# Kernel tuning notes

Hardware: AMD Instinct MI355X
Metric: run time of the kernel (lower is better)

Reference implementation:

```python
import jax, jax.numpy as jnp
import numpy as np
from jax import lax

B, N, NP, NS, CIN = 4, 8192, 2048, 32, 64
RADIUS = 0.1
CH = [CIN + 3, 64, 64, 128]  # mlp[0] += 3 because use_xyz=True
EPS = 1e-5


def _gather(x, idx):
    # x: [B, N, D], idx: [B, ...] int -> [B, ..., D]
    return jax.vmap(lambda a, i: a[i])(x, idx)


def _fps(xyz, npoint):
    # furthest point sampling, returns indices [B, npoint]
    b, n, _ = xyz.shape
    init_idx = jnp.zeros((b,), jnp.int32)
    dist0 = jnp.full((b, n), 1e10, xyz.dtype)

    def body(carry, _):
        dist, last = carry
        p = jnp.take_along_axis(xyz, last[:, None, None], axis=1)  # [B,1,3]
        d = jnp.sum((xyz - p) ** 2, axis=-1)                       # [B,N]
        dist = jnp.minimum(dist, d)
        nxt = jnp.argmax(dist, axis=-1).astype(jnp.int32)
        return (dist, nxt), nxt

    (_, _), rest = lax.scan(body, (dist0, init_idx), None, length=npoint - 1)
    return jnp.concatenate([init_idx[None, :], rest], axis=0).T    # [B, npoint]


def _ball_query(xyz, new_xyz, radius, nsample):
    # first `nsample` points within radius; pad with the first hit (0 if none)
    n = xyz.shape[1]
    d2 = jnp.sum((new_xyz[:, :, None, :] - xyz[:, None, :, :]) ** 2, axis=-1)  # [B,NP,N]
    score = jnp.where(d2 < radius * radius, jnp.arange(n, dtype=jnp.int32), n)
    neg_vals, _ = lax.top_k(-score, nsample)   # smallest indices first
    idx = -neg_vals                            # [B,NP,nsample]
    first = idx[..., :1]
    fill = jnp.where(first >= n, 0, first)
    return jnp.where(idx >= n, fill, idx)


def setup_inputs() -> dict:
    key = jax.random.key(0)
    ks = jax.random.split(key, 16)
    inp = {
        "xyz": jax.random.uniform(ks[0], (B, N, 3), jnp.float32),
        "features": jax.random.normal(ks[1], (B, CIN, N), jnp.float32),
    }
    for i in range(3):
        ci, co = CH[i], CH[i + 1]
        inp[f"W{i}"] = jax.random.normal(ks[2 + 4 * i], (co, ci), jnp.float32) / np.sqrt(ci)
        inp[f"b{i}"] = jnp.zeros((co,), jnp.float32)
        inp[f"g{i}"] = jnp.ones((co,), jnp.float32)
        inp[f"beta{i}"] = jnp.zeros((co,), jnp.float32)
    return inp


def _forward(xyz, features, params):
    fps_idx = _fps(xyz, NP)
    new_xyz = _gather(xyz, fps_idx)                                 # [B,NP,3]
    idx = _ball_query(xyz, new_xyz, RADIUS, NS)                     # [B,NP,NS]
    g_xyz = _gather(xyz, idx) - new_xyz[:, :, None, :]              # relative xyz
    g_feat = _gather(jnp.swapaxes(features, 1, 2), idx)             # [B,NP,NS,CIN]
    h = jnp.concatenate([g_xyz, g_feat], axis=-1)                   # [B,NP,NS,3+CIN]
    for (W, b, g, be) in params:
        h = jnp.einsum('bpsc,oc->bpso', h, W) + b                   # 1x1 conv
        mu = jnp.mean(h, axis=(0, 1, 2))
        var = jnp.var(h, axis=(0, 1, 2))
        h = (h - mu) * lax.rsqrt(var + EPS) * g + be                # BatchNorm2d (batch stats)
        h = jax.nn.relu(h)
    new_features = jnp.max(h, axis=2)                               # max-pool over nsample
    return new_xyz, jnp.swapaxes(new_features, 1, 2)                # [B,Cout,NP]


def reference(xyz, features, W0, b0, g0, beta0, W1, b1, g1, beta1, W2, b2, g2, beta2):
    params = ((W0, b0, g0, beta0), (W1, b1, g1, beta1), (W2, b2, g2, beta2))
    return _forward(xyz, features, params)
```

## Files before the change

kernel.cpp:

```cpp
#include <hip/hip_runtime.h>
#include <hip/hip_bf16.h>
#include <cstdint>

#define B_   4
#define N_   8192
#define NP_  2048
#define NS_  32
#define CIN_ 64
#define M_   (B_*NP_*NS_)
#define EPS_ 1e-5f
#define R2_  0.01f

typedef unsigned long long ull;
typedef float v2f __attribute__((ext_vector_type(2)));

__global__ __launch_bounds__(256) void transpose_kernel(const float* __restrict__ feat,
                                                        __hip_bfloat16* __restrict__ featT)
{
    __shared__ float tile[64][65];
    const int b  = blockIdx.y;
    const int j0 = blockIdx.x * 64;
    const int tx = threadIdx.x & 63, ty = threadIdx.x >> 6;
    for (int cc = ty; cc < 64; cc += 4)
        tile[tx][cc] = feat[((size_t)(b*CIN_ + cc))*N_ + j0 + tx];
    __syncthreads();
    for (int cc = ty; cc < 64; cc += 4)
        featT[((size_t)(b*N_ + j0 + cc))*64 + tx] = __float2bfloat16(tile[cc][tx]);
}

template<int CTRL>
__device__ __forceinline__ float dppmaxf(float v)
{
    int o = __builtin_amdgcn_update_dpp(__float_as_int(v), __float_as_int(v), CTRL, 0xF, 0xF, false);
    return fmaxf(v, __int_as_float(o));
}

__global__ __launch_bounds__(512) void fps_kernel(const float* __restrict__ xyz,
    int* __restrict__ fps_idx, float* __restrict__ new_xyzf, float* __restrict__ out)
{
#pragma clang fp contract(off)
    const int b = blockIdx.x;
    const int t = threadIdx.x;
    const float* X = xyz + (size_t)b * N_ * 3;

    __shared__ float xs[N_], ys[N_], zs[N_];
    __shared__ float wavemax[8];
    __shared__ unsigned widx_slot[2];

    for (int p = t; p < N_; p += 512) {
        xs[p] = X[p*3+0]; ys[p] = X[p*3+1]; zs[p] = X[p*3+2];
    }
    if (t < 2) widx_slot[t] = 0u;

    v2f px[8], py[8], pz[8], dst[8];
#pragma unroll
    for (int g = 0; g < 8; ++g) {
        const int p0 = (2*g)*512 + t, p1 = (2*g+1)*512 + t;
        px[g] = (v2f){X[p0*3+0], X[p1*3+0]};
        py[g] = (v2f){X[p0*3+1], X[p1*3+1]};
        pz[g] = (v2f){X[p0*3+2], X[p1*3+2]};
        dst[g] = (v2f){1e10f, 1e10f};
    }
    const int wv = t >> 6, ln = t & 63;

    float cx = X[0], cy = X[1], cz = X[2];
    if (t == 0) {
        fps_idx[b*NP_] = 0;
        size_t o3 = (size_t)(b*NP_) * 3;
        new_xyzf[o3] = cx; new_xyzf[o3+1] = cy; new_xyzf[o3+2] = cz;
        out[o3] = cx; out[o3+1] = cy; out[o3+2] = cz;
    }
    for (int it = 1; it < NP_; ++it) {
        const int par = it & 1;
        float bestv = -1.0f;
        const v2f c0 = (v2f){cx, cx}, c1 = (v2f){cy, cy}, c2 = (v2f){cz, cz};
#pragma unroll
        for (int g = 0; g < 8; ++g) {
            v2f dx = px[g] - c0, dy = py[g] - c1, dz = pz[g] - c2;
            v2f dd = dx*dx;
            dd = dd + dy*dy;
            dd = dd + dz*dz;
            v2f nd;
            nd.x = fminf(dst[g].x, dd.x);
            nd.y = fminf(dst[g].y, dd.y);
            dst[g] = nd;
            bestv = fmaxf(bestv, nd.x);
            bestv = fmaxf(bestv, nd.y);
        }
        float wm = bestv;
        wm = dppmaxf<0x111>(wm);
        wm = dppmaxf<0x112>(wm);
        wm = dppmaxf<0x114>(wm);
        wm = dppmaxf<0x118>(wm);
        wm = dppmaxf<0x142>(wm);
        wm = dppmaxf<0x143>(wm);
        if (ln == 63) wavemax[wv] = wm;
        __syncthreads();
        if (t == 0) widx_slot[par ^ 1] = 0u;
        float bmax = fmaxf(fmaxf(fmaxf(wavemax[0], wavemax[1]), fmaxf(wavemax[2], wavemax[3])),
                           fmaxf(fmaxf(wavemax[4], wavemax[5]), fmaxf(wavemax[6], wavemax[7])));
        if (bestv == bmax) {
            unsigned nin = 0u;
#pragma unroll
            for (int g = 7; g >= 0; --g) {
                if (dst[g].y == bmax) nin = ~(unsigned)((2*g+1)*512 + t);
                if (dst[g].x == bmax) nin = ~(unsigned)((2*g)*512 + t);
            }
            atomicMax(&widx_slot[par], nin);
        }
        __syncthreads();
        const int widx = (int)(~widx_slot[par]);
        cx = xs[widx]; cy = ys[widx]; cz = zs[widx];
        if (t == 0) {
            fps_idx[b*NP_ + it] = widx;
            size_t o3 = ((size_t)(b*NP_ + it)) * 3;
            new_xyzf[o3] = cx; new_xyzf[o3+1] = cy; new_xyzf[o3+2] = cz;
            out[o3] = cx; out[o3+1] = cy; out[o3+2] = cz;
        }
    }
}

__global__ __launch_bounds__(256) void ball_kernel(const float* __restrict__ xyz,
    const float* __restrict__ new_xyzf, int* __restrict__ ballidx)
{
#pragma clang fp contract(off)
    const int gw   = (blockIdx.x * 256 + threadIdx.x) >> 6;
    const int lane = threadIdx.x & 63;
    const int b    = gw >> 11;
    const float* X = xyz + (size_t)b * N_ * 3;
    const float cx = new_xyzf[(size_t)gw*3];
    const float cy = new_xyzf[(size_t)gw*3+1];
    const float cz = new_xyzf[(size_t)gw*3+2];
    int* outp = ballidx + (size_t)gw * NS_;
    int total = 0, first = -1;
    for (int base = 0; base < N_; base += 64) {
        const int j = base + lane;
        float dx = cx - X[j*3], dy = cy - X[j*3+1], dz = cz - X[j*3+2];
        float d2 = dx*dx;
        d2 = d2 + dy*dy;
        d2 = d2 + dz*dz;
        const bool in = d2 <= R2_;
        ull m = __ballot(in);
        if (m) {
            if (first < 0) first = base + __builtin_ctzll(m);
            int r = total + __popcll(m & ((1ull << lane) - 1ull));
            if (in && r < NS_) outp[r] = j;
            total += (int)__popcll(m);
            if (total >= NS_) break;
        }
    }
    if (total < NS_) {
        int f = first < 0 ? 0 : first;
        if (lane >= total && lane < NS_) outp[lane] = f;
    }
}

__global__ __launch_bounds__(256) void gemm1_kernel(const float* __restrict__ xyz,
    const __hip_bfloat16* __restrict__ featT, const float* __restrict__ newxyz,
    const int* __restrict__ ballidx, const float* __restrict__ W, const float* __restrict__ bias,
    __hip_bfloat16* __restrict__ pre1, float* __restrict__ psum, float* __restrict__ psumsq)
{
    const int lane = threadIdx.x & 63;
    const int gw   = (blockIdx.x * 256 + threadIdx.x) >> 6;
    float w[67];
#pragma unroll
    for (int k = 0; k < 67; ++k) w[k] = W[lane*67 + k];
    const float bs = bias[lane];
    float s1 = 0.f, s2 = 0.f;
    for (int r = gw; r < M_; r += 4096) {
        const int b = r >> 16;
        const int p = (r & 65535) >> 5;
        const int j = ballidx[r];
        const float* xp = xyz    + ((size_t)b*N_  + j)*3;
        const float* cp = newxyz + ((size_t)b*NP_ + p)*3;
        float acc = bs;
        acc = fmaf(xp[0] - cp[0], w[0], acc);
        acc = fmaf(xp[1] - cp[1], w[1], acc);
        acc = fmaf(xp[2] - cp[2], w[2], acc);
        const uint4* rp = (const uint4*)(featT + ((size_t)b*N_ + j)*64);
#pragma unroll
        for (int q = 0; q < 8; ++q) {
            const uint4 u4 = rp[q];
            const unsigned uu0 = u4.x, uu1 = u4.y, uu2 = u4.z, uu3 = u4.w;
            acc = fmaf(__uint_as_float(uu0 << 16),         w[3 + q*8 + 0], acc);
            acc = fmaf(__uint_as_float(uu0 & 0xffff0000u), w[3 + q*8 + 1], acc);
            acc = fmaf(__uint_as_float(uu1 << 16),         w[3 + q*8 + 2], acc);
            acc = fmaf(__uint_as_float(uu1 & 0xffff0000u), w[3 + q*8 + 3], acc);
            acc = fmaf(__uint_as_float(uu2 << 16),         w[3 + q*8 + 4], acc);
            acc = fmaf(__uint_as_float(uu2 & 0xffff0000u), w[3 + q*8 + 5], acc);
            acc = fmaf(__uint_as_float(uu3 << 16),         w[3 + q*8 + 6], acc);
            acc = fmaf(__uint_as_float(uu3 & 0xffff0000u), w[3 + q*8 + 7], acc);
        }
        pre1[(size_t)r*64 + lane] = __float2bfloat16(acc);
        s1 += acc;
        s2 = fmaf(acc, acc, s2);
    }
    psum  [(size_t)gw*64 + lane] = s1;
    psumsq[(size_t)gw*64 + lane] = s2;
}

__global__ __launch_bounds__(256) void epi_kernel(__hip_bfloat16* __restrict__ buf,
    const float* __restrict__ sc, const float* __restrict__ sh)
{
    __shared__ float ssc[64], ssh[64];
    if (threadIdx.x < 64) { ssc[threadIdx.x] = sc[threadIdx.x]; ssh[threadIdx.x] = sh[threadIdx.x]; }
    __syncthreads();
    const size_t idx = (size_t)blockIdx.x * 256 + threadIdx.x;
    const int k0 = (threadIdx.x & 7) * 8;
    uint4* p = (uint4*)buf;
    uint4 u = p[idx];
    unsigned wds[4] = {u.x, u.y, u.z, u.w};
    unsigned res[4];
#pragma unroll
    for (int m = 0; m < 4; ++m) {
        const int k = k0 + m*2;
        float v0 = __uint_as_float(wds[m] << 16);
        float v1 = __uint_as_float(wds[m] & 0xffff0000u);
        v0 = fmaxf(fmaf(v0, ssc[k],   ssh[k]),   0.f);
        v1 = fmaxf(fmaf(v1, ssc[k+1], ssh[k+1]), 0.f);
        __hip_bfloat16 b0 = __float2bfloat16(v0);
        __hip_bfloat16 b1 = __float2bfloat16(v1);
        unsigned short s0 = *reinterpret_cast<unsigned short*>(&b0);
        unsigned short s1 = *reinterpret_cast<unsigned short*>(&b1);
        res[m] = (unsigned)s0 | ((unsigned)s1 << 16);
    }
    p[idx] = make_uint4(res[0], res[1], res[2], res[3]);
}

__global__ __launch_bounds__(256) void gemm2_kernel(__hip_bfloat16* __restrict__ buf,
    const float* __restrict__ W, const float* __restrict__ bias,
    float* __restrict__ psum, float* __restrict__ psumsq)
{
    const int lane = threadIdx.x & 63;
    const int gw   = (blockIdx.x * 256 + threadIdx.x) >> 6;
    float w[64];
#pragma unroll
    for (int k = 0; k < 64; ++k) w[k] = W[lane*64 + k];
    const float bs = bias[lane];
    float s1 = 0.f, s2 = 0.f;
    for (int r = gw; r < M_; r += 4096) {
        const uint4* rp = (const uint4*)(buf + (size_t)r*64);
        float acc = bs;
#pragma unroll
        for (int q = 0; q < 8; ++q) {
            const uint4 u4 = rp[q];
            const unsigned uu0 = u4.x, uu1 = u4.y, uu2 = u4.z, uu3 = u4.w;
            acc = fmaf(__uint_as_float(uu0 << 16),         w[q*8 + 0], acc);
            acc = fmaf(__uint_as_float(uu0 & 0xffff0000u), w[q*8 + 1], acc);
            acc = fmaf(__uint_as_float(uu1 << 16),         w[q*8 + 2], acc);
            acc = fmaf(__uint_as_float(uu1 & 0xffff0000u), w[q*8 + 3], acc);
            acc = fmaf(__uint_as_float(uu2 << 16),         w[q*8 + 4], acc);
            acc = fmaf(__uint_as_float(uu2 & 0xffff0000u), w[q*8 + 5], acc);
            acc = fmaf(__uint_as_float(uu3 << 16),         w[q*8 + 6], acc);
            acc = fmaf(__uint_as_float(uu3 & 0xffff0000u), w[q*8 + 7], acc);
        }
        buf[(size_t)r*64 + lane] = __float2bfloat16(acc);
        s1 += acc;
        s2 = fmaf(acc, acc, s2);
    }
    psum  [(size_t)gw*64 + lane] = s1;
    psumsq[(size_t)gw*64 + lane] = s2;
}

__global__ __launch_bounds__(256) void gemm3_kernel(const __hip_bfloat16* __restrict__ act2,
    const float* __restrict__ W, const float* __restrict__ bias,
    float* __restrict__ mxb, float* __restrict__ mnb,
    float* __restrict__ psum, float* __restrict__ psumsq)
{
    const int lane = threadIdx.x & 63;
    const int gw   = (blockIdx.x * 256 + threadIdx.x) >> 6;
    const int pt   = gw >> 1;
    const int half = gw & 1;
    const int o = half*64 + lane;
    float w[64];
#pragma unroll
    for (int k = 0; k < 64; ++k) w[k] = W[o*64 + k];
    const float bs = bias[o];
    float s1 = 0.f, s2 = 0.f, mx = -1e30f, mn = 1e30f;
    for (int s = 0; s < NS_; ++s) {
        const size_t r = (size_t)pt*NS_ + s;
        const uint4* rp = (const uint4*)(act2 + r*64);
        float acc = bs;
#pragma unroll
        for (int q = 0; q < 8; ++q) {
            const uint4 u4 = rp[q];
            const unsigned uu0 = u4.x, uu1 = u4.y, uu2 = u4.z, uu3 = u4.w;
            acc = fmaf(__uint_as_float(uu0 << 16),         w[q*8 + 0], acc);
            acc = fmaf(__uint_as_float(uu0 & 0xffff0000u), w[q*8 + 1], acc);
            acc = fmaf(__uint_as_float(uu1 << 16),         w[q*8 + 2], acc);
            acc = fmaf(__uint_as_float(uu1 & 0xffff0000u), w[q*8 + 3], acc);
            acc = fmaf(__uint_as_float(uu2 << 16),         w[q*8 + 4], acc);
            acc = fmaf(__uint_as_float(uu2 & 0xffff0000u), w[q*8 + 5], acc);
            acc = fmaf(__uint_as_float(uu3 << 16),         w[q*8 + 6], acc);
            acc = fmaf(__uint_as_float(uu3 & 0xffff0000u), w[q*8 + 7], acc);
        }
        s1 += acc;
        s2 = fmaf(acc, acc, s2);
        mx = fmaxf(mx, acc);
        mn = fminf(mn, acc);
    }
    mxb[(size_t)pt*128 + o] = mx;
    mnb[(size_t)pt*128 + o] = mn;
    psum  [(size_t)pt*128 + o] = s1;
    psumsq[(size_t)pt*128 + o] = s2;
}

template<int CO>
__global__ __launch_bounds__(256) void bnred_kernel(const float* __restrict__ psum,
    const float* __restrict__ psumsq, const float* __restrict__ g, const float* __restrict__ beta,
    float* __restrict__ sc, float* __restrict__ sh, int nslots)
{
    const int c = blockIdx.x;
    const int t = threadIdx.x;
    float s1 = 0, s2 = 0;
    for (int i = t; i < nslots; i += 256) {
        s1 += psum  [(size_t)i*CO + c];
        s2 += psumsq[(size_t)i*CO + c];
    }
    __shared__ float a1[256], a2[256];
    a1[t] = s1; a2[t] = s2;
    __syncthreads();
    for (int st = 128; st > 0; st >>= 1) {
        if (t < st) { a1[t] += a1[t+st]; a2[t] += a2[t+st]; }
        __syncthreads();
    }
    if (t == 0) {
        const float invM = 1.0f / (float)M_;
        float mu  = a1[0] * invM;
        float var = fmaxf(a2[0] * invM - mu*mu, 0.f);
        float rs  = 1.0f / sqrtf(var + EPS_);
        float s   = rs * g[c];
        sc[c] = s;
        sh[c] = fmaf(-mu, s, beta[c]);
    }
}

__global__ __launch_bounds__(256) void final_kernel(const float* __restrict__ mxb,
    const float* __restrict__ mnb, const float* __restrict__ sc, const float* __restrict__ sh,
    float* __restrict__ out)
{
    __shared__ float tile[128][65];
    const int b = blockIdx.y, p0 = blockIdx.x * 64;
    {
        const int o = threadIdx.x & 127, ph = threadIdx.x >> 7;
        const float s = sc[o], h = sh[o];
        const bool pos = (s >= 0.f);
        for (int pl = ph; pl < 64; pl += 2) {
            const size_t pt = (size_t)b*NP_ + p0 + pl;
            float v = pos ? mxb[pt*128 + o] : mnb[pt*128 + o];
            tile[o][pl] = fmaxf(fmaf(v, s, h), 0.f);
        }
    }
    __syncthreads();
    {
        const int p = threadIdx.x & 63, oh = threadIdx.x >> 6;
        for (int oo = oh; oo < 128; oo += 4)
            out[(size_t)(B_*NP_*3) + ((size_t)(b*128 + oo))*NP_ + p0 + p] = tile[oo][p];
    }
}

extern "C" void kernel_launch(void* const* d_in, const int* in_sizes, int n_in,
                              void* d_out, int out_size, void* d_ws, size_t ws_size,
                              hipStream_t stream)
{
    const float* xyz  = (const float*)d_in[0];
    const float* feat = (const float*)d_in[1];
    const float* W0   = (const float*)d_in[2];
    const float* b0   = (const float*)d_in[3];
    const float* g0   = (const float*)d_in[4];
    const float* be0  = (const float*)d_in[5];
    const float* W1   = (const float*)d_in[6];
    const float* b1   = (const float*)d_in[7];
    const float* g1   = (const float*)d_in[8];
    const float* be1  = (const float*)d_in[9];
    const float* W2   = (const float*)d_in[10];
    const float* b2   = (const float*)d_in[11];
    const float* g2   = (const float*)d_in[12];
    const float* be2  = (const float*)d_in[13];

    char* ws = (char*)d_ws;
    int*   fpsidx = (int*)  (ws + 0);
    float* newxyz = (float*)(ws + 32768);
    int*   ball   = (int*)  (ws + 131072);
    float* scb    = (float*)(ws + 1179648);
    float* psum   = (float*)(ws + 1183744);
    float* psumsq = (float*)(ws + 5378048);
    __hip_bfloat16* featT = (__hip_bfloat16*)(ws + 9572352);
    float* mxb    = (float*)(ws + 13766656);
    float* mnb    = (float*)(ws + 17960960);
    __hip_bfloat16* buf1 = (__hip_bfloat16*)(ws + 22155264);
    float* out = (float*)d_out;

    float* sc1 = scb;       float* sh1 = scb + 128;
    float* sc2 = scb + 256; float* sh2 = scb + 384;
    float* sc3 = scb + 512; float* sh3 = scb + 640;

    transpose_kernel<<<dim3(N_/64, B_), 256, 0, stream>>>(feat, featT);
    fps_kernel<<<dim3(B_), 512, 0, stream>>>(xyz, fpsidx, newxyz, out);
    ball_kernel<<<dim3(B_*NP_/4), 256, 0, stream>>>(xyz, newxyz, ball);

    gemm1_kernel<<<1024, 256, 0, stream>>>(xyz, featT, newxyz, ball, W0, b0, buf1, psum, psumsq);
    bnred_kernel<64><<<64, 256, 0, stream>>>(psum, psumsq, g0, be0, sc1, sh1, 4096);
    epi_kernel<<<M_*64/8/256, 256, 0, stream>>>(buf1, sc1, sh1);
    gemm2_kernel<<<1024, 256, 0, stream>>>(buf1, W1, b1, psum, psumsq);
    bnred_kernel<64><<<64, 256, 0, stream>>>(psum, psumsq, g1, be1, sc2, sh2, 4096);
    epi_kernel<<<M_*64/8/256, 256, 0, stream>>>(buf1, sc2, sh2);
    gemm3_kernel<<<4096, 256, 0, stream>>>(buf1, W2, b2, mxb, mnb, psum, psumsq);
    bnred_kernel<128><<<128, 256, 0, stream>>>(psum, psumsq, g2, be2, sc3, sh3, 8192);
    final_kernel<<<dim3(NP_/64, B_), 256, 0, stream>>>(mxb, mnb, sc3, sh3, out);
}
```

Before: 2.381 ms.

## Use a single-barrier FPS argmax with packed 64-bit atomic key

The per-iteration FPS reduction changes from two block barriers plus a shared wave-max array to a single barrier. Each wave's winning lane does an atomicMax on one 64-bit key that packs the iteration number, the distance bits and the inverted index. Putting the iteration in the high bits means the slot never needs resetting, and the index bits keep ties resolved to the lowest index. Point coordinates move into a float4 shared array, and the global writes of the sampled points are deferred to after the loop using a shared index list. In exchange it relies on 64-bit LDS atomics and drops the unused fps_idx output.

```diff
diff --git a/kernel.cpp b/kernel.cpp
--- a/kernel.cpp
+++ b/kernel.cpp
@@ -36,21 +36,20 @@
 }
 
 __global__ __launch_bounds__(512) void fps_kernel(const float* __restrict__ xyz,
-    int* __restrict__ fps_idx, float* __restrict__ new_xyzf, float* __restrict__ out)
+    float* __restrict__ new_xyzf, float* __restrict__ out)
 {
 #pragma clang fp contract(off)
     const int b = blockIdx.x;
     const int t = threadIdx.x;
     const float* X = xyz + (size_t)b * N_ * 3;
 
-    __shared__ float xs[N_], ys[N_], zs[N_];
-    __shared__ float wavemax[8];
-    __shared__ unsigned widx_slot[2];
-
-    for (int p = t; p < N_; p += 512) {
-        xs[p] = X[p*3+0]; ys[p] = X[p*3+1]; zs[p] = X[p*3+2];
-    }
-    if (t < 2) widx_slot[t] = 0u;
+    __shared__ float4 xyz4[N_];
+    __shared__ unsigned short widxs[NP_];
+    __shared__ ull slot;
+
+    for (int p = t; p < N_; p += 512)
+        xyz4[p] = make_float4(X[p*3+0], X[p*3+1], X[p*3+2], 0.f);
+    if (t == 0) { slot = 0ull; widxs[0] = 0; }
 
     v2f px[8], py[8], pz[8], dst[8];
 #pragma unroll
@@ -61,17 +60,10 @@
         pz[g] = (v2f){X[p0*3+2], X[p1*3+2]};
         dst[g] = (v2f){1e10f, 1e10f};
     }
-    const int wv = t >> 6, ln = t & 63;
-
     float cx = X[0], cy = X[1], cz = X[2];
-    if (t == 0) {
-        fps_idx[b*NP_] = 0;
-        size_t o3 = (size_t)(b*NP_) * 3;
-        new_xyzf[o3] = cx; new_xyzf[o3+1] = cy; new_xyzf[o3+2] = cz;
-        out[o3] = cx; out[o3+1] = cy; out[o3+2] = cz;
-    }
+    __syncthreads();
+
     for (int it = 1; it < NP_; ++it) {
-        const int par = it & 1;
         float bestv = -1.0f;
         const v2f c0 = (v2f){cx, cx}, c1 = (v2f){cy, cy}, c2 = (v2f){cz, cz};
 #pragma unroll
@@ -94,29 +86,32 @@
         wm = dppmaxf<0x118>(wm);
         wm = dppmaxf<0x142>(wm);
         wm = dppmaxf<0x143>(wm);
-        if (ln == 63) wavemax[wv] = wm;
+        const float wm_b = __int_as_float(__builtin_amdgcn_readlane(__float_as_int(wm), 63));
+        if (bestv == wm_b) {
+            int idx = 0;
+#pragma unroll
+            for (int g = 7; g >= 0; --g) {
+                if (dst[g].y == wm_b) idx = (2*g+1)*512 + t;
+                if (dst[g].x == wm_b) idx = (2*g)*512 + t;
+            }
+            const ull key = ((ull)(unsigned)it << 45)
+                          | ((ull)__float_as_uint(wm_b) << 13)
+                          | (ull)(unsigned)(8191 - idx);
+            atomicMax(&slot, key);
+        }
         __syncthreads();
-        if (t == 0) widx_slot[par ^ 1] = 0u;
-        float bmax = fmaxf(fmaxf(fmaxf(wavemax[0], wavemax[1]), fmaxf(wavemax[2], wavemax[3])),
-                           fmaxf(fmaxf(wavemax[4], wavemax[5]), fmaxf(wavemax[6], wavemax[7])));
-        if (bestv == bmax) {
-            unsigned nin = 0u;
-#pragma unroll
-            for (int g = 7; g >= 0; --g) {
-                if (dst[g].y == bmax) nin = ~(unsigned)((2*g+1)*512 + t);
-                if (dst[g].x == bmax) nin = ~(unsigned)((2*g)*512 + t);
-            }
-            atomicMax(&widx_slot[par], nin);
-        }
-        __syncthreads();
-        const int widx = (int)(~widx_slot[par]);
-        cx = xs[widx]; cy = ys[widx]; cz = zs[widx];
-        if (t == 0) {
-            fps_idx[b*NP_ + it] = widx;
-            size_t o3 = ((size_t)(b*NP_ + it)) * 3;
-            new_xyzf[o3] = cx; new_xyzf[o3+1] = cy; new_xyzf[o3+2] = cz;
-            out[o3] = cx; out[o3+1] = cy; out[o3+2] = cz;
-        }
+        const ull k = slot;
+        const int widx = 8191 - (int)(k & 0x1fffull);
+        if (t == 0) widxs[it] = (unsigned short)widx;
+        const float4 c = xyz4[widx];
+        cx = c.x; cy = c.y; cz = c.z;
+    }
+    __syncthreads();
+    for (int i = t; i < NP_; i += 512) {
+        const float4 c = xyz4[widxs[i]];
+        const size_t o3 = ((size_t)(b*NP_ + i)) * 3;
+        new_xyzf[o3] = c.x; new_xyzf[o3+1] = c.y; new_xyzf[o3+2] = c.z;
+        out[o3] = c.x; out[o3+1] = c.y; out[o3+2] = c.z;
     }
 }
 
@@ -379,7 +374,6 @@
     const float* be2  = (const float*)d_in[13];
 
     char* ws = (char*)d_ws;
-    int*   fpsidx = (int*)  (ws + 0);
     float* newxyz = (float*)(ws + 32768);
     int*   ball   = (int*)  (ws + 131072);
     float* scb    = (float*)(ws + 1179648);
@@ -396,7 +390,7 @@
     float* sc3 = scb + 512; float* sh3 = scb + 640;
 
     transpose_kernel<<<dim3(N_/64, B_), 256, 0, stream>>>(feat, featT);
-    fps_kernel<<<dim3(B_), 512, 0, stream>>>(xyz, fpsidx, newxyz, out);
+    fps_kernel<<<dim3(B_), 512, 0, stream>>>(xyz, newxyz, out);
     ball_kernel<<<dim3(B_*NP_/4), 256, 0, stream>>>(xyz, newxyz, ball);
 
     gemm1_kernel<<<1024, 256, 0, stream>>>(xyz, featT, newxyz, ball, W0, b0, buf1, psum, psumsq);
```

New measurement: 2.597 ms. +9.1%, slower.
